# Kernel tuning notes

Measured on AMD Instinct MI355X. Metric: run time of the kernel, lower is better.

Reference implementation:

```python
import jax, jax.numpy as jnp
import numpy as np

B, T, C, H = 2, 2048, 1024, 16
D = C // H  # head dim = 64

def setup_inputs() -> dict:
    key = jax.random.key(0)
    k1, k2, k3 = jax.random.split(key, 3)
    x = jax.random.normal(k1, (B, T, C), dtype=jnp.float32)
    Wqkv = jax.random.normal(k2, (C, 3 * C), dtype=jnp.float32) * (1.0 / np.sqrt(C))
    bqkv = jnp.zeros((3 * C,), dtype=jnp.float32)
    Wproj = jax.random.normal(k3, (C, C), dtype=jnp.float32) * (1.0 / np.sqrt(C))
    bproj = jnp.zeros((C,), dtype=jnp.float32)
    return {"x": x, "Wqkv": Wqkv, "bqkv": bqkv, "Wproj": Wproj, "bproj": bproj}

def reference(x, Wqkv, bqkv, Wproj, bproj):
    b, t, c = x.shape
    qkv = x @ Wqkv + bqkv                      # [B,T,3C]
    q, k, v = jnp.split(qkv, 3, axis=-1)
    # [B,T,C] -> [B,H,T,D]
    def heads(y):
        return y.reshape(b, t, H, D).transpose(0, 2, 1, 3)
    q, k, v = heads(q), heads(k), heads(v)
    scale = 1.0 / np.sqrt(D)
    scores = jnp.einsum('bhqd,bhkd->bhqk', q, k) * scale  # [B,H,T,T]
    causal = jnp.tril(jnp.ones((t, t), dtype=bool))
    scores = jnp.where(causal, scores, jnp.finfo(scores.dtype).min)
    attn = jax.nn.softmax(scores, axis=-1)
    out = jnp.einsum('bhqk,bhkd->bhqd', attn, v)          # [B,H,T,D]
    out = out.transpose(0, 2, 1, 3).reshape(b, t, c)      # [B,T,C]
    return out @ Wproj + bproj
```

## Files before the change

kernel.cpp:

```cpp
#include <hip/hip_runtime.h>
#include <hip/hip_bf16.h>

#define B_ 2
#define T_ 2048
#define C_ 1024
#define H_ 16
#define D_ 64
#define M_ROWS (B_ * T_)
#define N_QKV (3 * C_)

typedef __bf16 bf16x8 __attribute__((ext_vector_type(8)));
typedef float f32x4 __attribute__((ext_vector_type(4)));

#define SC 0.18033688011112042f

__device__ __forceinline__ void gl_lds16(const __bf16* g, __bf16* l) {
    __builtin_amdgcn_global_load_lds(
        (const __attribute__((address_space(1))) unsigned int*)g,
        (__attribute__((address_space(3))) unsigned int*)l, 16, 0, 0);
}

__global__ __launch_bounds__(256) void conv_bf16(const float* __restrict__ in,
                                                 __bf16* __restrict__ out, int n8)
{
    int i = blockIdx.x * 256 + threadIdx.x;
    if (i >= n8) return;
    const float4* p = (const float4*)(in + (size_t)i * 8);
    float4 a = p[0], b = p[1];
    __bf16 v[8] = {(__bf16)a.x, (__bf16)a.y, (__bf16)a.z, (__bf16)a.w,
                   (__bf16)b.x, (__bf16)b.y, (__bf16)b.z, (__bf16)b.w};
    *(uint4*)(out + (size_t)i * 8) = *(uint4*)v;
}

__global__ __launch_bounds__(256) void transp_w(const float* __restrict__ W,
                                                __bf16* __restrict__ Wt, int K, int N)
{
    __shared__ __bf16 Ts[64 * 72];
    const int tid = threadIdx.x;
    const int k0 = blockIdx.x * 64, n0 = blockIdx.y * 64;
#pragma unroll
    for (int i = 0; i < 4; ++i) {
        int f = i * 256 + tid;
        int r = f >> 4, c4 = (f & 15) * 4;
        float4 v = *(const float4*)(W + (size_t)(k0 + r) * N + n0 + c4);
        Ts[(c4 + 0) * 72 + r] = (__bf16)v.x;
        Ts[(c4 + 1) * 72 + r] = (__bf16)v.y;
        Ts[(c4 + 2) * 72 + r] = (__bf16)v.z;
        Ts[(c4 + 3) * 72 + r] = (__bf16)v.w;
    }
    __syncthreads();
#pragma unroll
    for (int i = 0; i < 2; ++i) {
        int f = i * 256 + tid;
        int n = f >> 3, c8 = (f & 7) * 8;
        *(uint4*)(Wt + (size_t)(n0 + n) * K + k0 + c8) = *(const uint4*)&Ts[n * 72 + c8];
    }
}

__global__ __launch_bounds__(256) void transp_v(const __bf16* __restrict__ qkv,
                                                __bf16* __restrict__ vt)
{
    __shared__ __bf16 Ts[64 * 72];
    const int tid = threadIdx.x;
    const int gx = blockIdx.x, gy = blockIdx.y;
#pragma unroll
    for (int i = 0; i < 2; ++i) {
        int f = i * 256 + tid;
        int r = f >> 3, c8 = (f & 7) * 8;
        uint4 v = *(const uint4*)(qkv + (size_t)(gx * 64 + r) * N_QKV + 2 * C_ + gy * 64 + c8);
        const __bf16* vb = (const __bf16*)&v;
#pragma unroll
        for (int j = 0; j < 8; ++j) Ts[(c8 + j) * 72 + r] = vb[j];
    }
    __syncthreads();
    const int b = gx >> 5;
    const int tbase = (gx & 31) * 64;
#pragma unroll
    for (int i = 0; i < 2; ++i) {
        int f = i * 256 + tid;
        int c = f >> 3, t8 = (f & 7) * 8;
        *(uint4*)(vt + ((size_t)b * C_ + gy * 64 + c) * T_ + tbase + t8) =
            *(const uint4*)&Ts[c * 72 + t8];
    }
}

#define GBK 64

template <typename OT>
__global__ __launch_bounds__(256) void gemm_bt(
    const __bf16* __restrict__ A, const __bf16* __restrict__ Bt,
    const float* __restrict__ bias, OT* __restrict__ C,
    int M, int N, int K)
{
    __shared__ __bf16 As[128 * GBK];
    __shared__ __bf16 Bs[128 * GBK];

    const int tid  = threadIdx.x;
    const int m0   = blockIdx.x * 128;
    const int n0   = blockIdx.y * 128;
    const int w    = tid >> 6;
    const int lane = tid & 63;
    const int quad = lane >> 4;
    const int l16  = lane & 15;
    const int wr   = (w >> 1) * 64;
    const int wc   = (w & 1) * 64;

    const int srow = w * 32 + (lane >> 3);
    const int sseg = ((lane & 7) ^ (lane >> 3)) * 8;
    const __bf16* Ag = A + (size_t)(m0 + srow) * K + sseg;
    const __bf16* Bg = Bt + (size_t)(n0 + srow) * K + sseg;

    f32x4 acc[4][4] = {};

    for (int k0 = 0; k0 < K; k0 += GBK) {
#pragma unroll
        for (int i = 0; i < 4; ++i) {
            gl_lds16(Ag + k0 + (size_t)(i * 8) * K, &As[(w * 32 + i * 8) * GBK]);
            gl_lds16(Bg + k0 + (size_t)(i * 8) * K, &Bs[(w * 32 + i * 8) * GBK]);
        }
        __syncthreads();
#pragma unroll
        for (int kk = 0; kk < 2; ++kk) {
            bf16x8 af[4], bf[4];
#pragma unroll
            for (int mi = 0; mi < 4; ++mi)
                af[mi] = *(const bf16x8*)&As[(wr + mi * 16 + l16) * GBK +
                                             (((kk * 4 + quad) ^ (l16 & 7)) * 8)];
#pragma unroll
            for (int ni = 0; ni < 4; ++ni)
                bf[ni] = *(const bf16x8*)&Bs[(wc + ni * 16 + l16) * GBK +
                                             (((kk * 4 + quad) ^ (l16 & 7)) * 8)];
#pragma unroll
            for (int mi = 0; mi < 4; ++mi)
#pragma unroll
                for (int ni = 0; ni < 4; ++ni)
                    acc[mi][ni] = __builtin_amdgcn_mfma_f32_16x16x32_bf16(
                        af[mi], bf[ni], acc[mi][ni], 0, 0, 0);
        }
        __syncthreads();
    }

#pragma unroll
    for (int mi = 0; mi < 4; ++mi) {
#pragma unroll
        for (int ni = 0; ni < 4; ++ni) {
            int col = n0 + wc + ni * 16 + l16;
            float bv = bias[col];
#pragma unroll
            for (int r = 0; r < 4; ++r) {
                int row = m0 + wr + mi * 16 + quad * 4 + r;
                C[(size_t)row * N + col] = (OT)(acc[mi][ni][r] + bv);
            }
        }
    }
}

__global__ __launch_bounds__(256) void attn_kernel(
    const __bf16* __restrict__ qkv, const __bf16* __restrict__ vt,
    __bf16* __restrict__ out)
{
    __shared__ __bf16 Qs[64 * 64];
    __shared__ __bf16 KVs[4][64 * 64];
    __shared__ __bf16 Ps[4][16 * 64];

    const int tid  = threadIdx.x;
    const int p    = blockIdx.x;
    const int bh   = blockIdx.y;
    const int b    = bh >> 4;
    const int h    = bh & 15;
    const int w    = tid >> 6;
    const int lane = tid & 63;
    const int quad = lane >> 4;
    const int l16  = lane & 15;
    const int lxor = l16 & 7;

    const int srow = lane >> 3;
    const int sseg = ((lane & 7) ^ srow) * 8;
    __bf16* Psw = &Ps[w][0];

    for (int half = 0; half < 2; ++half) {
        const int qt = half ? (31 - p) : p;

        {
            const __bf16* Qg = qkv + (size_t)(b * T_ + qt * 64 + w * 16 + srow) * N_QKV
                             + (size_t)h * 64 + sseg;
            gl_lds16(Qg, &Qs[(w * 16) * 64]);
            gl_lds16(Qg + (size_t)8 * N_QKV, &Qs[(w * 16 + 8) * 64]);
            const __bf16* Kg = qkv + (size_t)(b * T_ + w * 16 + srow) * N_QKV
                             + C_ + (size_t)h * 64 + sseg;
            gl_lds16(Kg, &KVs[0][(w * 16) * 64]);
            gl_lds16(Kg + (size_t)8 * N_QKV, &KVs[0][(w * 16 + 8) * 64]);
            const __bf16* Vg = vt + ((size_t)(b * H_ + h) * 64 + w * 16 + srow) * T_ + sseg;
            gl_lds16(Vg, &KVs[1][(w * 16) * 64]);
            gl_lds16(Vg + (size_t)8 * T_, &KVs[1][(w * 16 + 8) * 64]);
        }
        __syncthreads();

        bf16x8 qf[2];
#pragma unroll
        for (int kk = 0; kk < 2; ++kk)
            qf[kk] = *(const bf16x8*)&Qs[(w * 16 + l16) * 64 + (((kk * 4 + quad) ^ lxor) * 8)];

        f32x4 o[4] = {};
        float lacc = 0.f;

        for (int kt = 0; kt <= qt; ++kt) {
            const __bf16* Ks = KVs[(kt & 1) * 2];
            const __bf16* Vs = KVs[(kt & 1) * 2 + 1];

            if (kt < qt) {
                int nb = ((kt + 1) & 1) * 2;
                const __bf16* Kg = qkv + (size_t)(b * T_ + (kt + 1) * 64 + w * 16 + srow) * N_QKV
                                 + C_ + (size_t)h * 64 + sseg;
                gl_lds16(Kg, &KVs[nb][(w * 16) * 64]);
                gl_lds16(Kg + (size_t)8 * N_QKV, &KVs[nb][(w * 16 + 8) * 64]);
                const __bf16* Vg = vt + ((size_t)(b * H_ + h) * 64 + w * 16 + srow) * T_
                                 + (kt + 1) * 64 + sseg;
                gl_lds16(Vg, &KVs[nb + 1][(w * 16) * 64]);
                gl_lds16(Vg + (size_t)8 * T_, &KVs[nb + 1][(w * 16 + 8) * 64]);
            }

            f32x4 s[4] = {};
#pragma unroll
            for (int ni = 0; ni < 4; ++ni) {
#pragma unroll
                for (int kk = 0; kk < 2; ++kk) {
                    bf16x8 kf = *(const bf16x8*)&Ks[(ni * 16 + l16) * 64 +
                                                    (((kk * 4 + quad) ^ lxor) * 8)];
                    s[ni] = __builtin_amdgcn_mfma_f32_16x16x32_bf16(kf, qf[kk], s[ni], 0, 0, 0);
                }
            }

            if (kt == qt) {
#pragma unroll
                for (int ni = 0; ni < 4; ++ni)
#pragma unroll
                    for (int r = 0; r < 4; ++r)
                        if (ni * 16 + quad * 4 + r > w * 16 + l16) s[ni][r] = -3.0e38f;
            }

#pragma unroll
            for (int ni = 0; ni < 4; ++ni) {
                __bf16 pb[4];
#pragma unroll
                for (int r = 0; r < 4; ++r) {
                    float pe = __builtin_amdgcn_exp2f(s[ni][r] * SC);
                    lacc += pe;
                    pb[r] = (__bf16)pe;
                }
                int seg = (ni * 2 + (quad >> 1)) ^ lxor;
                *(uint2*)&Psw[l16 * 64 + seg * 8 + (quad & 1) * 4] = *(uint2*)pb;
            }
            __threadfence_block();

            bf16x8 pf[2];
#pragma unroll
            for (int kk = 0; kk < 2; ++kk)
                pf[kk] = *(const bf16x8*)&Psw[l16 * 64 + (((kk * 4 + quad) ^ lxor) * 8)];
#pragma unroll
            for (int ni = 0; ni < 4; ++ni) {
#pragma unroll
                for (int kk = 0; kk < 2; ++kk) {
                    bf16x8 vf = *(const bf16x8*)&Vs[(ni * 16 + l16) * 64 +
                                                    (((kk * 4 + quad) ^ lxor) * 8)];
                    o[ni] = __builtin_amdgcn_mfma_f32_16x16x32_bf16(pf[kk], vf, o[ni], 0, 0, 0);
                }
            }
            __syncthreads();
        }

        lacc += __shfl_xor(lacc, 16, 64);
        lacc += __shfl_xor(lacc, 32, 64);

#pragma unroll
        for (int r = 0; r < 4; ++r) {
            float linv = 1.f / __shfl(lacc, quad * 4 + r, 64);
            int trow = qt * 64 + w * 16 + quad * 4 + r;
#pragma unroll
            for (int ni = 0; ni < 4; ++ni)
                out[((size_t)(b * T_ + trow)) * C_ + h * 64 + ni * 16 + l16] =
                    (__bf16)(o[ni][r] * linv);
        }
    }
}

extern "C" void kernel_launch(void* const* d_in, const int* in_sizes, int n_in,
                              void* d_out, int out_size, void* d_ws, size_t ws_size,
                              hipStream_t stream)
{
    const float* x     = (const float*)d_in[0];
    const float* Wqkv  = (const float*)d_in[1];
    const float* bqkv  = (const float*)d_in[2];
    const float* Wproj = (const float*)d_in[3];
    const float* bproj = (const float*)d_in[4];
    float* out = (float*)d_out;

    char* ws = (char*)d_ws;
    __bf16* xb     = (__bf16*)(ws);
    __bf16* Wqkvt  = (__bf16*)(ws + (8u << 20));
    __bf16* Wprojt = (__bf16*)(ws + (14u << 20));
    __bf16* qkv    = (__bf16*)(ws + (16u << 20));
    __bf16* vt     = (__bf16*)(ws + (40u << 20));
    __bf16* att    = xb;

    conv_bf16<<<(M_ROWS * C_ / 8 + 255) / 256, 256, 0, stream>>>(x, xb, M_ROWS * C_ / 8);
    transp_w<<<dim3(C_ / 64, N_QKV / 64), 256, 0, stream>>>(Wqkv, Wqkvt, C_, N_QKV);
    transp_w<<<dim3(C_ / 64, C_ / 64), 256, 0, stream>>>(Wproj, Wprojt, C_, C_);

    gemm_bt<__bf16><<<dim3(M_ROWS / 128, N_QKV / 128), 256, 0, stream>>>(
        xb, Wqkvt, bqkv, qkv, M_ROWS, N_QKV, C_);

    transp_v<<<dim3(M_ROWS / 64, C_ / 64), 256, 0, stream>>>(qkv, vt);

    attn_kernel<<<dim3(16, B_ * H_), 256, 0, stream>>>(qkv, vt, att);

    gemm_bt<float><<<dim3(M_ROWS / 128, C_ / 128), 256, 0, stream>>>(
        att, Wprojt, bproj, out, M_ROWS, C_, C_);
}
```

Measured before the change: 187.1 us.

## Fuse V transpose into QKV GEMM epilogue and widen attention query tiles

The QKV GEMM epilogue now writes Q/K to a compact buffer and V directly in transposed layout, which removes the separate transp_v kernel. The two weight-transpose launches are merged into one. The attention kernel now processes 128 query rows per block as two 64-row groups that share each K/V tile load, halving K/V traffic per query. Its grid is reordered to 32x16, with heavy tiles scheduled first. The V epilogue stores are strided 8-byte writes, and the larger per-block state raises register and LDS use.

```diff
diff --git a/kernel.cpp b/kernel.cpp
--- a/kernel.cpp
+++ b/kernel.cpp
@@ -8,6 +8,7 @@
 #define D_ 64
 #define M_ROWS (B_ * T_)
 #define N_QKV (3 * C_)
+#define QKS (2 * C_)
 
 typedef __bf16 bf16x8 __attribute__((ext_vector_type(8)));
 typedef float f32x4 __attribute__((ext_vector_type(4)));
@@ -32,12 +33,17 @@
     *(uint4*)(out + (size_t)i * 8) = *(uint4*)v;
 }
 
-__global__ __launch_bounds__(256) void transp_w(const float* __restrict__ W,
-                                                __bf16* __restrict__ Wt, int K, int N)
+__global__ __launch_bounds__(256) void transp_w2(
+    const float* __restrict__ Wqkv, const float* __restrict__ Wproj,
+    __bf16* __restrict__ Wqkvt, __bf16* __restrict__ Wprojt)
 {
     __shared__ __bf16 Ts[64 * 72];
     const int tid = threadIdx.x;
-    const int k0 = blockIdx.x * 64, n0 = blockIdx.y * 64;
+    const int gy = blockIdx.y;
+    const float* W; __bf16* Wt; int N, n0;
+    if (gy < 48) { W = Wqkv;  Wt = Wqkvt;  N = N_QKV; n0 = gy * 64; }
+    else         { W = Wproj; Wt = Wprojt; N = C_;    n0 = (gy - 48) * 64; }
+    const int k0 = blockIdx.x * 64;
 #pragma unroll
     for (int i = 0; i < 4; ++i) {
         int f = i * 256 + tid;
@@ -53,44 +59,16 @@
     for (int i = 0; i < 2; ++i) {
         int f = i * 256 + tid;
         int n = f >> 3, c8 = (f & 7) * 8;
-        *(uint4*)(Wt + (size_t)(n0 + n) * K + k0 + c8) = *(const uint4*)&Ts[n * 72 + c8];
-    }
-}
-
-__global__ __launch_bounds__(256) void transp_v(const __bf16* __restrict__ qkv,
-                                                __bf16* __restrict__ vt)
-{
-    __shared__ __bf16 Ts[64 * 72];
-    const int tid = threadIdx.x;
-    const int gx = blockIdx.x, gy = blockIdx.y;
-#pragma unroll
-    for (int i = 0; i < 2; ++i) {
-        int f = i * 256 + tid;
-        int r = f >> 3, c8 = (f & 7) * 8;
-        uint4 v = *(const uint4*)(qkv + (size_t)(gx * 64 + r) * N_QKV + 2 * C_ + gy * 64 + c8);
-        const __bf16* vb = (const __bf16*)&v;
-#pragma unroll
-        for (int j = 0; j < 8; ++j) Ts[(c8 + j) * 72 + r] = vb[j];
-    }
-    __syncthreads();
-    const int b = gx >> 5;
-    const int tbase = (gx & 31) * 64;
-#pragma unroll
-    for (int i = 0; i < 2; ++i) {
-        int f = i * 256 + tid;
-        int c = f >> 3, t8 = (f & 7) * 8;
-        *(uint4*)(vt + ((size_t)b * C_ + gy * 64 + c) * T_ + tbase + t8) =
-            *(const uint4*)&Ts[c * 72 + t8];
+        *(uint4*)(Wt + (size_t)(n0 + n) * C_ + k0 + c8) = *(const uint4*)&Ts[n * 72 + c8];
     }
 }
 
 #define GBK 64
 
-template <typename OT>
-__global__ __launch_bounds__(256) void gemm_bt(
+__global__ __launch_bounds__(256) void gemm_qkv(
     const __bf16* __restrict__ A, const __bf16* __restrict__ Bt,
-    const float* __restrict__ bias, OT* __restrict__ C,
-    int M, int N, int K)
+    const float* __restrict__ bias, __bf16* __restrict__ qk,
+    __bf16* __restrict__ vt)
 {
     __shared__ __bf16 As[128 * GBK];
     __shared__ __bf16 Bs[128 * GBK];
@@ -104,6 +82,7 @@
     const int l16  = lane & 15;
     const int wr   = (w >> 1) * 64;
     const int wc   = (w & 1) * 64;
+    const int K = C_, N = N_QKV;
 
     const int srow = w * 32 + (lane >> 3);
     const int sseg = ((lane & 7) ^ (lane >> 3)) * 8;
@@ -140,6 +119,94 @@
         __syncthreads();
     }
 
+    if (n0 < 2 * C_) {
+#pragma unroll
+        for (int mi = 0; mi < 4; ++mi) {
+#pragma unroll
+            for (int ni = 0; ni < 4; ++ni) {
+                int col = n0 + wc + ni * 16 + l16;
+                float bv = bias[col];
+#pragma unroll
+                for (int r = 0; r < 4; ++r) {
+                    int row = m0 + wr + mi * 16 + quad * 4 + r;
+                    qk[(size_t)row * QKS + col] = (__bf16)(acc[mi][ni][r] + bv);
+                }
+            }
+        }
+    } else {
+        const int bb = m0 >> 11;
+        const int tb = (m0 & (T_ - 1)) + wr;
+#pragma unroll
+        for (int mi = 0; mi < 4; ++mi) {
+#pragma unroll
+            for (int ni = 0; ni < 4; ++ni) {
+                int col = n0 + wc + ni * 16 + l16;
+                float bv = bias[col];
+                int c = col - 2 * C_;
+                int t0 = tb + mi * 16 + quad * 4;
+                __bf16 pb[4];
+#pragma unroll
+                for (int r = 0; r < 4; ++r)
+                    pb[r] = (__bf16)(acc[mi][ni][r] + bv);
+                *(uint2*)&vt[((size_t)bb * C_ + c) * T_ + t0] = *(uint2*)pb;
+            }
+        }
+    }
+}
+
+__global__ __launch_bounds__(256) void gemm_proj(
+    const __bf16* __restrict__ A, const __bf16* __restrict__ Bt,
+    const float* __restrict__ bias, float* __restrict__ C)
+{
+    __shared__ __bf16 As[128 * GBK];
+    __shared__ __bf16 Bs[128 * GBK];
+
+    const int tid  = threadIdx.x;
+    const int m0   = blockIdx.x * 128;
+    const int n0   = blockIdx.y * 128;
+    const int w    = tid >> 6;
+    const int lane = tid & 63;
+    const int quad = lane >> 4;
+    const int l16  = lane & 15;
+    const int wr   = (w >> 1) * 64;
+    const int wc   = (w & 1) * 64;
+    const int K = C_, N = C_;
+
+    const int srow = w * 32 + (lane >> 3);
+    const int sseg = ((lane & 7) ^ (lane >> 3)) * 8;
+    const __bf16* Ag = A + (size_t)(m0 + srow) * K + sseg;
+    const __bf16* Bg = Bt + (size_t)(n0 + srow) * K + sseg;
+
+    f32x4 acc[4][4] = {};
+
+    for (int k0 = 0; k0 < K; k0 += GBK) {
+#pragma unroll
+        for (int i = 0; i < 4; ++i) {
+            gl_lds16(Ag + k0 + (size_t)(i * 8) * K, &As[(w * 32 + i * 8) * GBK]);
+            gl_lds16(Bg + k0 + (size_t)(i * 8) * K, &Bs[(w * 32 + i * 8) * GBK]);
+        }
+        __syncthreads();
+#pragma unroll
+        for (int kk = 0; kk < 2; ++kk) {
+            bf16x8 af[4], bf[4];
+#pragma unroll
+            for (int mi = 0; mi < 4; ++mi)
+                af[mi] = *(const bf16x8*)&As[(wr + mi * 16 + l16) * GBK +
+                                             (((kk * 4 + quad) ^ (l16 & 7)) * 8)];
+#pragma unroll
+            for (int ni = 0; ni < 4; ++ni)
+                bf[ni] = *(const bf16x8*)&Bs[(wc + ni * 16 + l16) * GBK +
+                                             (((kk * 4 + quad) ^ (l16 & 7)) * 8)];
+#pragma unroll
+            for (int mi = 0; mi < 4; ++mi)
+#pragma unroll
+                for (int ni = 0; ni < 4; ++ni)
+                    acc[mi][ni] = __builtin_amdgcn_mfma_f32_16x16x32_bf16(
+                        af[mi], bf[ni], acc[mi][ni], 0, 0, 0);
+        }
+        __syncthreads();
+    }
+
 #pragma unroll
     for (int mi = 0; mi < 4; ++mi) {
 #pragma unroll
@@ -149,23 +216,24 @@
 #pragma unroll
             for (int r = 0; r < 4; ++r) {
                 int row = m0 + wr + mi * 16 + quad * 4 + r;
-                C[(size_t)row * N + col] = (OT)(acc[mi][ni][r] + bv);
+                C[(size_t)row * N + col] = acc[mi][ni][r] + bv;
             }
         }
     }
 }
 
 __global__ __launch_bounds__(256) void attn_kernel(
-    const __bf16* __restrict__ qkv, const __bf16* __restrict__ vt,
+    const __bf16* __restrict__ qk, const __bf16* __restrict__ vt,
     __bf16* __restrict__ out)
 {
-    __shared__ __bf16 Qs[64 * 64];
+    __shared__ __bf16 Qs[128 * 64];
     __shared__ __bf16 KVs[4][64 * 64];
-    __shared__ __bf16 Ps[4][16 * 64];
+    __shared__ __bf16 Ps[4][2][16 * 64];
 
     const int tid  = threadIdx.x;
-    const int p    = blockIdx.x;
-    const int bh   = blockIdx.y;
+    const int bh   = blockIdx.x;
+    const int j    = blockIdx.y;
+    const int qt   = (j < 8) ? (15 - j) : (j - 8);
     const int b    = bh >> 4;
     const int h    = bh & 15;
     const int w    = tid >> 6;
@@ -176,50 +244,54 @@
 
     const int srow = lane >> 3;
     const int sseg = ((lane & 7) ^ srow) * 8;
-    __bf16* Psw = &Ps[w][0];
-
-    for (int half = 0; half < 2; ++half) {
-        const int qt = half ? (31 - p) : p;
-
-        {
-            const __bf16* Qg = qkv + (size_t)(b * T_ + qt * 64 + w * 16 + srow) * N_QKV
-                             + (size_t)h * 64 + sseg;
-            gl_lds16(Qg, &Qs[(w * 16) * 64]);
-            gl_lds16(Qg + (size_t)8 * N_QKV, &Qs[(w * 16 + 8) * 64]);
-            const __bf16* Kg = qkv + (size_t)(b * T_ + w * 16 + srow) * N_QKV
+    const int nkt  = 2 * qt + 2;
+
+    {
+        const __bf16* Qg = qk + (size_t)(b * T_ + qt * 128 + w * 32 + srow) * QKS
+                         + (size_t)h * 64 + sseg;
+#pragma unroll
+        for (int i = 0; i < 4; ++i)
+            gl_lds16(Qg + (size_t)(i * 8) * QKS, &Qs[(w * 32 + i * 8) * 64]);
+        const __bf16* Kg = qk + (size_t)(b * T_ + w * 16 + srow) * QKS
+                         + C_ + (size_t)h * 64 + sseg;
+        gl_lds16(Kg, &KVs[0][(w * 16) * 64]);
+        gl_lds16(Kg + (size_t)8 * QKS, &KVs[0][(w * 16 + 8) * 64]);
+        const __bf16* Vg = vt + ((size_t)(b * H_ + h) * 64 + w * 16 + srow) * T_ + sseg;
+        gl_lds16(Vg, &KVs[1][(w * 16) * 64]);
+        gl_lds16(Vg + (size_t)8 * T_, &KVs[1][(w * 16 + 8) * 64]);
+    }
+    __syncthreads();
+
+    bf16x8 qf[2][2];
+#pragma unroll
+    for (int g = 0; g < 2; ++g)
+#pragma unroll
+        for (int kk = 0; kk < 2; ++kk)
+            qf[g][kk] = *(const bf16x8*)&Qs[(g * 64 + w * 16 + l16) * 64 +
+                                            (((kk * 4 + quad) ^ lxor) * 8)];
+
+    f32x4 o[2][4] = {};
+    float lacc[2] = {0.f, 0.f};
+
+    for (int kt = 0; kt < nkt; ++kt) {
+        const __bf16* Ks = KVs[(kt & 1) * 2];
+        const __bf16* Vs = KVs[(kt & 1) * 2 + 1];
+
+        if (kt + 1 < nkt) {
+            int nb = ((kt + 1) & 1) * 2;
+            const __bf16* Kg = qk + (size_t)(b * T_ + (kt + 1) * 64 + w * 16 + srow) * QKS
                              + C_ + (size_t)h * 64 + sseg;
-            gl_lds16(Kg, &KVs[0][(w * 16) * 64]);
-            gl_lds16(Kg + (size_t)8 * N_QKV, &KVs[0][(w * 16 + 8) * 64]);
-            const __bf16* Vg = vt + ((size_t)(b * H_ + h) * 64 + w * 16 + srow) * T_ + sseg;
-            gl_lds16(Vg, &KVs[1][(w * 16) * 64]);
-            gl_lds16(Vg + (size_t)8 * T_, &KVs[1][(w * 16 + 8) * 64]);
-        }
-        __syncthreads();
-
-        bf16x8 qf[2];
-#pragma unroll
-        for (int kk = 0; kk < 2; ++kk)
-            qf[kk] = *(const bf16x8*)&Qs[(w * 16 + l16) * 64 + (((kk * 4 + quad) ^ lxor) * 8)];
-
-        f32x4 o[4] = {};
-        float lacc = 0.f;
-
-        for (int kt = 0; kt <= qt; ++kt) {
-            const __bf16* Ks = KVs[(kt & 1) * 2];
-            const __bf16* Vs = KVs[(kt & 1) * 2 + 1];
-
-            if (kt < qt) {
-                int nb = ((kt + 1) & 1) * 2;
-                const __bf16* Kg = qkv + (size_t)(b * T_ + (kt + 1) * 64 + w * 16 + srow) * N_QKV
-                                 + C_ + (size_t)h * 64 + sseg;
-                gl_lds16(Kg, &KVs[nb][(w * 16) * 64]);
-                gl_lds16(Kg + (size_t)8 * N_QKV, &KVs[nb][(w * 16 + 8) * 64]);
-                const __bf16* Vg = vt + ((size_t)(b * H_ + h) * 64 + w * 16 + srow) * T_
-                                 + (kt + 1) * 64 + sseg;
-                gl_lds16(Vg, &KVs[nb + 1][(w * 16) * 64]);
-                gl_lds16(Vg + (size_t)8 * T_, &KVs[nb + 1][(w * 16 + 8) * 64]);
-            }
-
+            gl_lds16(Kg, &KVs[nb][(w * 16) * 64]);
+            gl_lds16(Kg + (size_t)8 * QKS, &KVs[nb][(w * 16 + 8) * 64]);
+            const __bf16* Vg = vt + ((size_t)(b * H_ + h) * 64 + w * 16 + srow) * T_
+                             + (kt + 1) * 64 + sseg;
+            gl_lds16(Vg, &KVs[nb + 1][(w * 16) * 64]);
+            gl_lds16(Vg + (size_t)8 * T_, &KVs[nb + 1][(w * 16 + 8) * 64]);
+        }
+
+#pragma unroll
+        for (int g = 0; g < 2; ++g) {
+            if (g == 0 && kt == nkt - 1) continue;
             f32x4 s[4] = {};
 #pragma unroll
             for (int ni = 0; ni < 4; ++ni) {
@@ -227,59 +299,65 @@
                 for (int kk = 0; kk < 2; ++kk) {
                     bf16x8 kf = *(const bf16x8*)&Ks[(ni * 16 + l16) * 64 +
                                                     (((kk * 4 + quad) ^ lxor) * 8)];
-                    s[ni] = __builtin_amdgcn_mfma_f32_16x16x32_bf16(kf, qf[kk], s[ni], 0, 0, 0);
+                    s[ni] = __builtin_amdgcn_mfma_f32_16x16x32_bf16(kf, qf[g][kk], s[ni], 0, 0, 0);
                 }
             }
-
-            if (kt == qt) {
+            if (kt == 2 * qt + g) {
 #pragma unroll
                 for (int ni = 0; ni < 4; ++ni)
 #pragma unroll
                     for (int r = 0; r < 4; ++r)
                         if (ni * 16 + quad * 4 + r > w * 16 + l16) s[ni][r] = -3.0e38f;
             }
-
+            __bf16* Psw = &Ps[w][g][0];
+            float la = 0.f;
 #pragma unroll
             for (int ni = 0; ni < 4; ++ni) {
                 __bf16 pb[4];
 #pragma unroll
                 for (int r = 0; r < 4; ++r) {
                     float pe = __builtin_amdgcn_exp2f(s[ni][r] * SC);
-                    lacc += pe;
+                    la += pe;
                     pb[r] = (__bf16)pe;
                 }
                 int seg = (ni * 2 + (quad >> 1)) ^ lxor;
                 *(uint2*)&Psw[l16 * 64 + seg * 8 + (quad & 1) * 4] = *(uint2*)pb;
             }
-            __threadfence_block();
-
-            bf16x8 pf[2];
-#pragma unroll
-            for (int kk = 0; kk < 2; ++kk)
-                pf[kk] = *(const bf16x8*)&Psw[l16 * 64 + (((kk * 4 + quad) ^ lxor) * 8)];
-#pragma unroll
-            for (int ni = 0; ni < 4; ++ni) {
-#pragma unroll
-                for (int kk = 0; kk < 2; ++kk) {
-                    bf16x8 vf = *(const bf16x8*)&Vs[(ni * 16 + l16) * 64 +
-                                                    (((kk * 4 + quad) ^ lxor) * 8)];
-                    o[ni] = __builtin_amdgcn_mfma_f32_16x16x32_bf16(pf[kk], vf, o[ni], 0, 0, 0);
+            lacc[g] += la;
+        }
+        __threadfence_block();
+
+#pragma unroll
+        for (int ni = 0; ni < 4; ++ni) {
+#pragma unroll
+            for (int kk = 0; kk < 2; ++kk) {
+                bf16x8 vf = *(const bf16x8*)&Vs[(ni * 16 + l16) * 64 +
+                                                (((kk * 4 + quad) ^ lxor) * 8)];
+#pragma unroll
+                for (int g = 0; g < 2; ++g) {
+                    if (g == 0 && kt == nkt - 1) continue;
+                    bf16x8 pf = *(const bf16x8*)&Ps[w][g][l16 * 64 +
+                                                        (((kk * 4 + quad) ^ lxor) * 8)];
+                    o[g][ni] = __builtin_amdgcn_mfma_f32_16x16x32_bf16(pf, vf, o[g][ni], 0, 0, 0);
                 }
             }
-            __syncthreads();
-        }
-
-        lacc += __shfl_xor(lacc, 16, 64);
-        lacc += __shfl_xor(lacc, 32, 64);
-
+        }
+        __syncthreads();
+    }
+
+#pragma unroll
+    for (int g = 0; g < 2; ++g) {
+        float la = lacc[g];
+        la += __shfl_xor(la, 16, 64);
+        la += __shfl_xor(la, 32, 64);
 #pragma unroll
         for (int r = 0; r < 4; ++r) {
-            float linv = 1.f / __shfl(lacc, quad * 4 + r, 64);
-            int trow = qt * 64 + w * 16 + quad * 4 + r;
+            float linv = 1.f / __shfl(la, quad * 4 + r, 64);
+            int trow = qt * 128 + g * 64 + w * 16 + quad * 4 + r;
 #pragma unroll
             for (int ni = 0; ni < 4; ++ni)
                 out[((size_t)(b * T_ + trow)) * C_ + h * 64 + ni * 16 + l16] =
-                    (__bf16)(o[ni][r] * linv);
+                    (__bf16)(o[g][ni][r] * linv);
         }
     }
 }
@@ -297,23 +375,20 @@
 
     char* ws = (char*)d_ws;
     __bf16* xb     = (__bf16*)(ws);
-    __bf16* Wqkvt  = (__bf16*)(ws + (8u << 20));
+    __bf16* Wqkvt  = (__bf16*)(ws + (8u  << 20));
     __bf16* Wprojt = (__bf16*)(ws + (14u << 20));
-    __bf16* qkv    = (__bf16*)(ws + (16u << 20));
-    __bf16* vt     = (__bf16*)(ws + (40u << 20));
+    __bf16* qk     = (__bf16*)(ws + (16u << 20));
+    __bf16* vt     = (__bf16*)(ws + (32u << 20));
     __bf16* att    = xb;
 
     conv_bf16<<<(M_ROWS * C_ / 8 + 255) / 256, 256, 0, stream>>>(x, xb, M_ROWS * C_ / 8);
-    transp_w<<<dim3(C_ / 64, N_QKV / 64), 256, 0, stream>>>(Wqkv, Wqkvt, C_, N_QKV);
-    transp_w<<<dim3(C_ / 64, C_ / 64), 256, 0, stream>>>(Wproj, Wprojt, C_, C_);
-
-    gemm_bt<__bf16><<<dim3(M_ROWS / 128, N_QKV / 128), 256, 0, stream>>>(
-        xb, Wqkvt, bqkv, qkv, M_ROWS, N_QKV, C_);
-
-    transp_v<<<dim3(M_ROWS / 64, C_ / 64), 256, 0, stream>>>(qkv, vt);
-
-    attn_kernel<<<dim3(16, B_ * H_), 256, 0, stream>>>(qkv, vt, att);
-
-    gemm_bt<float><<<dim3(M_ROWS / 128, C_ / 128), 256, 0, stream>>>(
-        att, Wprojt, bproj, out, M_ROWS, C_, C_);
-}
+    transp_w2<<<dim3(16, 64), 256, 0, stream>>>(Wqkv, Wproj, Wqkvt, Wprojt);
+
+    gemm_qkv<<<dim3(M_ROWS / 128, N_QKV / 128), 256, 0, stream>>>(
+        xb, Wqkvt, bqkv, qk, vt);
+
+    attn_kernel<<<dim3(32, 16), 256, 0, stream>>>(qk, vt, att);
+
+    gemm_proj<<<dim3(M_ROWS / 128, C_ / 128), 256, 0, stream>>>(
+        att, Wprojt, bproj, out);
+}
```

Measured after the change: 192.1 us. 1.03x slower.
